# Kernel optimization log

Hardware: AMD Instinct MI355X
Metric: run time of the kernel (lower is better)

The kernel has to match this reference:

```python
import jax, jax.numpy as jnp
import numpy as np
from jax import lax

DN = ('NCHW', 'OIHW', 'NCHW')


def _conv(x, w, pad):
    return lax.conv_general_dilated(x, w, (1, 1), [(pad, pad), (pad, pad)], dimension_numbers=DN)


def _bn(x, gamma, beta, mean, var, eps=1e-5):
    inv = gamma * lax.rsqrt(var + eps)
    return x * inv[None, :, None, None] + (beta - mean * inv)[None, :, None, None]


def _unfold(x, K, pad):
    # torch.nn.Unfold layout: channel-major, kernel positions fastest -> (B, C, K*K, H, W)
    B, C, H, W = x.shape
    p = lax.conv_general_dilated_patches(x, (K, K), (1, 1), [(pad, pad), (pad, pad)], dimension_numbers=DN)
    return p.reshape(B, C, K * K, H, W)


def setup_inputs() -> dict:
    key = jax.random.key(0)
    ks = jax.random.split(key, 16)
    B, C, H, W, K = 16, 64, 64, 64, 3
    d = {
        'x': jax.random.normal(ks[0], (B, C, H, W), jnp.float32),
        'wq': jax.random.normal(ks[1], (C, C, 1, 1), jnp.float32) * 0.1,
        'wk': jax.random.normal(ks[2], (C, C, K, K), jnp.float32) * 0.05,
        'wv': jax.random.normal(ks[3], (C, C, 1, 1), jnp.float32) * 0.1,
        'pos_h': jax.random.normal(ks[4], (C, K, 1), jnp.float32),
        'pos_w': jax.random.normal(ks[5], (C, 1, K), jnp.float32),
    }
    for i, nm in enumerate(['q', 'k', 'v', 'o']):
        d[nm + '_gamma'] = jnp.ones((C,), jnp.float32)
        d[nm + '_beta'] = jnp.zeros((C,), jnp.float32)
        d[nm + '_mean'] = jax.random.normal(ks[6 + i], (C,), jnp.float32) * 0.1
        d[nm + '_var'] = jax.random.uniform(ks[10 + i], (C,), jnp.float32, 0.5, 1.5)
    return d


def reference(x, wq, q_gamma, q_beta, q_mean, q_var,
              wk, k_gamma, k_beta, k_mean, k_var,
              wv, v_gamma, v_beta, v_mean, v_var,
              pos_h, pos_w, o_gamma, o_beta, o_mean, o_var):
    B, C, H, W = x.shape
    K = pos_h.shape[1]
    heads = C // 8
    cph = C // heads  # channels per head

    q = jax.nn.relu(_bn(_conv(x, wq, 0), q_gamma, q_beta, q_mean, q_var))
    k = jax.nn.relu(_bn(_conv(x, wk, K // 2), k_gamma, k_beta, k_mean, k_var))
    v = _bn(_conv(x, wv, 0), v_gamma, v_beta, v_mean, v_var)

    # local keys + positional bias: (B, C, K*K, H, W)
    unfold_k = _unfold(k, K, K // 2)
    pos = (pos_h + pos_w).reshape(1, C, K * K, 1, 1)
    kp = (unfold_k + pos).reshape(B, heads, cph, K * K, H, W)
    qh = q.reshape(B, heads, cph, 1, H, W)

    attn = (qh * kp).sum(axis=2)            # (B, heads, K*K, H, W)
    attn = jax.nn.softmax(attn, axis=2)

    # local aggregation (LocalConvolution): weights shared across cph channels per head
    uv = _unfold(v, K, (K - 1) // 2).reshape(B, heads, cph, K * K, H, W)
    out = (attn[:, :, None] * uv).sum(axis=3).reshape(B, C, H, W)

    out = jax.nn.relu(_bn(out, o_gamma, o_beta, o_mean, o_var))
    return out
```

## Files before the change

### kernel.cpp

```cpp
#include <hip/hip_runtime.h>
#include <hip/hip_bf16.h>
#include <math.h>

#define B_ 16
#define C_ 64
#define H_ 64
#define W_ 64
#define KSTEPS 18

typedef __attribute__((ext_vector_type(8))) short bf16x8;
typedef __attribute__((ext_vector_type(4))) short bf16x4;
typedef __attribute__((ext_vector_type(4))) float f32x4;

static __device__ __forceinline__ unsigned short f2b(float f) {
    __hip_bfloat16 h = __float2bfloat16(f);
    return *reinterpret_cast<unsigned short*>(&h);
}
static __device__ __forceinline__ float b2f(unsigned short u) {
    __hip_bfloat16 h;
    *reinterpret_cast<unsigned short*>(&h) = u;
    return __bfloat162float(h);
}

__global__ __launch_bounds__(64) void prep_kernel(
    const float* __restrict__ wq, const float* __restrict__ wk, const float* __restrict__ wv,
    const float* __restrict__ qg, const float* __restrict__ qb, const float* __restrict__ qm, const float* __restrict__ qv,
    const float* __restrict__ kg, const float* __restrict__ kb, const float* __restrict__ km, const float* __restrict__ kv,
    const float* __restrict__ vg, const float* __restrict__ vb, const float* __restrict__ vm, const float* __restrict__ vv,
    const float* __restrict__ og, const float* __restrict__ ob, const float* __restrict__ om, const float* __restrict__ ov,
    unsigned short* __restrict__ Wp, float* __restrict__ bnp)
{
    const int bid = blockIdx.x;
    const int lane = threadIdx.x;
    if (bid < 12 * KSTEPS) {
        const int mf = bid / KSTEPS;
        const int ks = bid % KSTEPS;
        const int r = lane & 15;
        bf16x8 u;
#pragma unroll
        for (int j = 0; j < 8; j++) {
            int k = ks * 32 + ((lane >> 4) << 3) + j;
            int tap = k >> 6;
            int c = k & 63;
            float w;
            if (mf < 4)      { int co = mf * 16 + r;        w = (tap == 4) ? wq[co * 64 + c] : 0.f; }
            else if (mf < 8) { int co = (mf - 4) * 16 + r;  w = wk[(co * 64 + c) * 9 + tap]; }
            else             { int co = (mf - 8) * 16 + r;  w = (tap == 4) ? wv[co * 64 + c] : 0.f; }
            u[j] = (short)f2b(w);
        }
        *reinterpret_cast<bf16x8*>(Wp + ((size_t)(mf * KSTEPS + ks) * 64 + lane) * 8) = u;
    } else {
        const int c = lane;
        const float* G[4] = {qg, kg, vg, og};
        const float* Bt[4] = {qb, kb, vb, ob};
        const float* M[4] = {qm, km, vm, om};
        const float* V[4] = {qv, kv, vv, ov};
#pragma unroll
        for (int p = 0; p < 4; p++) {
            float inv = G[p][c] * rsqrtf(V[p][c] + 1e-5f);
            bnp[p * 128 + c] = inv;
            bnp[p * 128 + 64 + c] = Bt[p][c] - M[p][c] * inv;
        }
    }
}

__global__ __launch_bounds__(256) void xt_kernel(
    const float* __restrict__ x, unsigned short* __restrict__ xt)
{
    __shared__ float ls[64][65];
    const int b = blockIdx.x >> 6;
    const int h = blockIdx.x & 63;
    const int tid = threadIdx.x;
    const int w = tid & 63;
    const int cg = tid >> 6;
#pragma unroll
    for (int cc = 0; cc < 16; cc++) {
        int c = cg * 16 + cc;
        ls[c][w] = x[((b * 64 + c) * 64 + h) * 64 + w];
    }
    __syncthreads();
    const int px = tid & 63;
    bf16x8 u0, u1;
#pragma unroll
    for (int j = 0; j < 8; j++) {
        u0[j] = (short)f2b(ls[cg * 16 + j][px]);
        u1[j] = (short)f2b(ls[cg * 16 + 8 + j][px]);
    }
    size_t base = ((size_t)((b * 64 + h) * 64 + px)) * 64 + cg * 16;
    *reinterpret_cast<bf16x8*>(xt + base) = u0;
    *reinterpret_cast<bf16x8*>(xt + base + 8) = u1;
}

#define KSM_OFF 0
#define VSM_OFF 25344
#define QSM_OFF 50688
__global__ __launch_bounds__(512, 2) void fused_kernel(
    const unsigned short* __restrict__ xt, const unsigned short* __restrict__ Wp,
    const float* __restrict__ bnp,
    const float* __restrict__ ph, const float* __restrict__ pw,
    float* __restrict__ out)
{
    __shared__ __align__(16) char smem[58880];
    __shared__ float bns[512];
    __shared__ float phs[192], pws[192];
    const int bid = blockIdx.x;
    const int b = bid >> 6;
    const int h = bid & 63;
    const int tid = threadIdx.x;

    for (int i = tid; i < 5 * 66 * 8; i += 512) {
        int ch  = i & 7;
        int col = (i >> 3) % 66;
        int dy  = (i >> 3) / 66;
        int gh = h - 2 + dy, gw = col - 1;
        bf16x8 u = (bf16x8){0,0,0,0,0,0,0,0};
        if ((unsigned)gh < 64u && (unsigned)gw < 64u)
            u = *reinterpret_cast<const bf16x8*>(xt + ((size_t)((b * 64 + gh) * 64 + gw)) * 64 + ch * 8);
        int La = ((dy * 66 + col) * 64 + ch * 8) * 2;
        La ^= (col & 7) << 4;
        *reinterpret_cast<bf16x8*>(smem + La) = u;
    }
    bns[tid & 511] = bnp[tid & 511];
    if (tid < 192) { phs[tid] = ph[tid]; pws[tid] = pw[tid]; }
    __syncthreads();

    const int wid = tid >> 6, lane = tid & 63;
    const int mf = wid & 3, half = wid >> 2;
    const int t = lane & 15, q4 = lane >> 4;
    const int qbase = half ? 0 : 4;

    f32x4 acck[6], accv[6], accq[2];
#pragma unroll
    for (int n = 0; n < 6; n++) { acck[n] = (f32x4){0.f,0.f,0.f,0.f}; accv[n] = (f32x4){0.f,0.f,0.f,0.f}; }
    accq[0] = (f32x4){0.f,0.f,0.f,0.f}; accq[1] = (f32x4){0.f,0.f,0.f,0.f};

#pragma unroll
    for (int ks = 0; ks < KSTEPS; ks++) {
        const int tap = ks >> 1;
        const int dy = tap / 3, dx = tap - dy * 3;
        const int kb = (ks & 1) * 32 + q4 * 8;
        bf16x8 bf[6];
#pragma unroll
        for (int n = 0; n < 6; n++) {
            int p = (half * 6 + n) * 16 + t;
            int r = p >> 6, colw = p & 63;
            int col = colw + dx;
            int La = (((r + dy) * 66 + col) * 64 + kb) * 2;
            La ^= (col & 7) << 4;
            bf[n] = *reinterpret_cast<const bf16x8*>(smem + La);
        }
        bf16x8 afk = *reinterpret_cast<const bf16x8*>(Wp + ((size_t)((4 + mf) * KSTEPS + ks) * 64 + lane) * 8);
#pragma unroll
        for (int n = 0; n < 6; n++)
            acck[n] = __builtin_amdgcn_mfma_f32_16x16x32_bf16(afk, bf[n], acck[n], 0, 0, 0);
        if (ks == 8 || ks == 9) {
            bf16x8 afq = *reinterpret_cast<const bf16x8*>(Wp + ((size_t)(mf * KSTEPS + ks) * 64 + lane) * 8);
            bf16x8 afv = *reinterpret_cast<const bf16x8*>(Wp + ((size_t)((8 + mf) * KSTEPS + ks) * 64 + lane) * 8);
#pragma unroll
            for (int n = 0; n < 6; n++)
                accv[n] = __builtin_amdgcn_mfma_f32_16x16x32_bf16(afv, bf[n], accv[n], 0, 0, 0);
            accq[0] = __builtin_amdgcn_mfma_f32_16x16x32_bf16(afq, bf[qbase], accq[0], 0, 0, 0);
            accq[1] = __builtin_amdgcn_mfma_f32_16x16x32_bf16(afq, bf[qbase + 1], accq[1], 0, 0, 0);
        }
    }
    __syncthreads();

    const int c0 = mf * 16 + q4 * 4;
    {
        f32x4 invk  = *reinterpret_cast<const f32x4*>(&bns[128 + c0]);
        f32x4 biask = *reinterpret_cast<const f32x4*>(&bns[128 + 64 + c0]);
        f32x4 invv  = *reinterpret_cast<const f32x4*>(&bns[256 + c0]);
        f32x4 biasv = *reinterpret_cast<const f32x4*>(&bns[256 + 64 + c0]);
#pragma unroll
        for (int n = 0; n < 6; n++) {
            int p = (half * 6 + n) * 16 + t;
            int r = p >> 6, colw = p & 63;
            int pxp = colw + 1;
            int La = ((r * 66 + pxp) * 64 + c0) * 2;
            La ^= (pxp & 7) << 4;
            bf16x4 pk, pv;
#pragma unroll
            for (int j = 0; j < 4; j++) {
                pk[j] = (short)f2b(fmaxf(acck[n][j] * invk[j] + biask[j], 0.f));
                pv[j] = (short)f2b(accv[n][j] * invv[j] + biasv[j]);
            }
            *reinterpret_cast<bf16x4*>(smem + KSM_OFF + La) = pk;
            *reinterpret_cast<bf16x4*>(smem + VSM_OFF + La) = pv;
        }
        f32x4 invq  = *reinterpret_cast<const f32x4*>(&bns[c0]);
        f32x4 biasq = *reinterpret_cast<const f32x4*>(&bns[64 + c0]);
#pragma unroll
        for (int i = 0; i < 2; i++) {
            int nq = 4 + half * 2 + i;
            int colw = (nq & 3) * 16 + t;
            int La = (colw * 64 + c0) * 2;
            La ^= (colw & 7) << 4;
            bf16x4 pq;
#pragma unroll
            for (int j = 0; j < 4; j++)
                pq[j] = (short)f2b(fmaxf(accq[i][j] * invq[j] + biasq[j], 0.f));
            *reinterpret_cast<bf16x4*>(smem + QSM_OFF + La) = pq;
        }
    }
    __syncthreads();

    const bf16x8 z8 = (bf16x8){0,0,0,0,0,0,0,0};
    for (int i = tid; i < 96; i += 512) {
        int buf = i & 1;
        int j = i >> 1;
        int ch = j & 7;
        int jj = j >> 3;
        int col = (jj & 1) ? 65 : 0;
        int rr = jj >> 1;
        int La = ((rr * 66 + col) * 64 + ch * 8) * 2;
        La ^= (col & 7) << 4;
        *reinterpret_cast<bf16x8*>(smem + (buf ? VSM_OFF : KSM_OFF) + La) = z8;
    }
    int rbad = (h == 0) ? 0 : ((h == 63) ? 2 : -1);
    if (rbad >= 0) {
        for (int i = tid; i < 66 * 8 * 2; i += 512) {
            int buf = i & 1;
            int j = i >> 1;
            int ch = j & 7;
            int col = j >> 3;
            int La = ((rbad * 66 + col) * 64 + ch * 8) * 2;
            La ^= (col & 7) << 4;
            *reinterpret_cast<bf16x8*>(smem + (buf ? VSM_OFF : KSM_OFF) + La) = z8;
        }
    }
    __syncthreads();

    const int px = tid & 63;
    const int head = tid >> 6;
    const int cb = head * 8;

    float qf[8];
    {
        int Lq = (px * 64 + cb) * 2;
        Lq ^= (px & 7) << 4;
        bf16x8 q8 = *reinterpret_cast<const bf16x8*>(smem + QSM_OFF + Lq);
#pragma unroll
        for (int j = 0; j < 8; j++) qf[j] = b2f((unsigned short)q8[j]);
    }

    float A[3], Bx[3];
#pragma unroll
    for (int tt = 0; tt < 3; tt++) {
        float a = 0.f, bb = 0.f;
#pragma unroll
        for (int j = 0; j < 8; j++) {
            a  = fmaf(qf[j], phs[(cb + j) * 3 + tt], a);
            bb = fmaf(qf[j], pws[(cb + j) * 3 + tt], bb);
        }
        A[tt] = a; Bx[tt] = bb;
    }

    float logit[9];
#pragma unroll
    for (int dy = 0; dy < 3; dy++) {
#pragma unroll
        for (int dx = 0; dx < 3; dx++) {
            int pxp = px + dx;
            int La = ((dy * 66 + pxp) * 64 + cb) * 2;
            La ^= (pxp & 7) << 4;
            bf16x8 k8 = *reinterpret_cast<const bf16x8*>(smem + KSM_OFF + La);
            float qk = 0.f;
#pragma unroll
            for (int j = 0; j < 8; j++) qk = fmaf(qf[j], b2f((unsigned short)k8[j]), qk);
            logit[dy * 3 + dx] = qk + A[dy] + Bx[dx];
        }
    }

    float mx = logit[0];
#pragma unroll
    for (int tt = 1; tt < 9; tt++) mx = fmaxf(mx, logit[tt]);
    float e[9], sum = 0.f;
#pragma unroll
    for (int tt = 0; tt < 9; tt++) { e[tt] = __expf(logit[tt] - mx); sum += e[tt]; }
    float inv = 1.f / sum;

    float o[8];
#pragma unroll
    for (int j = 0; j < 8; j++) o[j] = 0.f;
#pragma unroll
    for (int dy = 0; dy < 3; dy++) {
#pragma unroll
        for (int dx = 0; dx < 3; dx++) {
            int pxp = px + dx;
            int La = ((dy * 66 + pxp) * 64 + cb) * 2;
            La ^= (pxp & 7) << 4;
            bf16x8 v8 = *reinterpret_cast<const bf16x8*>(smem + VSM_OFF + La);
            float w = e[dy * 3 + dx];
#pragma unroll
            for (int j = 0; j < 8; j++) o[j] = fmaf(w, b2f((unsigned short)v8[j]), o[j]);
        }
    }

#pragma unroll
    for (int j = 0; j < 8; j++) {
        int c = cb + j;
        float val = fmaxf(fmaf(o[j] * inv, bns[384 + c], bns[384 + 64 + c]), 0.f);
        out[((size_t)(b * C_ + c) * H_ + h) * W_ + px] = val;
    }
}

extern "C" void kernel_launch(void* const* d_in, const int* in_sizes, int n_in,
                              void* d_out, int out_size, void* d_ws, size_t ws_size,
                              hipStream_t stream)
{
    const float* x   = (const float*)d_in[0];
    const float* wq  = (const float*)d_in[1];
    const float* wk  = (const float*)d_in[2];
    const float* wv  = (const float*)d_in[3];
    const float* ph  = (const float*)d_in[4];
    const float* pw  = (const float*)d_in[5];
    const float* qg  = (const float*)d_in[6];
    const float* qb  = (const float*)d_in[7];
    const float* qm  = (const float*)d_in[8];
    const float* qv  = (const float*)d_in[9];
    const float* kg  = (const float*)d_in[10];
    const float* kb  = (const float*)d_in[11];
    const float* km  = (const float*)d_in[12];
    const float* kv  = (const float*)d_in[13];
    const float* vg  = (const float*)d_in[14];
    const float* vb  = (const float*)d_in[15];
    const float* vm  = (const float*)d_in[16];
    const float* vv  = (const float*)d_in[17];
    const float* og  = (const float*)d_in[18];
    const float* ob  = (const float*)d_in[19];
    const float* om  = (const float*)d_in[20];
    const float* ov  = (const float*)d_in[21];

    char* ws = (char*)d_ws;
    unsigned short* Wp = (unsigned short*)ws;
    float* bnp = (float*)(ws + 221184);
    unsigned short* xt = (unsigned short*)(ws + 223232);

    prep_kernel<<<12 * KSTEPS + 1, 64, 0, stream>>>(
        wq, wk, wv, qg, qb, qm, qv, kg, kb, km, kv, vg, vb, vm, vv,
        og, ob, om, ov, Wp, bnp);

    xt_kernel<<<B_ * H_, 256, 0, stream>>>(x, xt);

    fused_kernel<<<B_ * H_, 512, 0, stream>>>(xt, Wp, bnp, ph, pw, (float*)d_out);
}
```

Baseline: 180.3 us.

## Switch shared-memory tiles to channel-chunk-major layout and raise occupancy hint

```diff
diff --git a/kernel.cpp b/kernel.cpp
--- a/kernel.cpp
+++ b/kernel.cpp
@@ -94,7 +94,7 @@
 #define KSM_OFF 0
 #define VSM_OFF 25344
 #define QSM_OFF 50688
-__global__ __launch_bounds__(512, 2) void fused_kernel(
+__global__ __launch_bounds__(512, 4) void fused_kernel(
     const unsigned short* __restrict__ xt, const unsigned short* __restrict__ Wp,
     const float* __restrict__ bnp,
     const float* __restrict__ ph, const float* __restrict__ pw,
@@ -108,17 +108,16 @@
     const int h = bid & 63;
     const int tid = threadIdx.x;
 
-    for (int i = tid; i < 5 * 66 * 8; i += 512) {
-        int ch  = i & 7;
-        int col = (i >> 3) % 66;
-        int dy  = (i >> 3) / 66;
+    for (int i = tid; i < 8 * 5 * 66; i += 512) {
+        int ch   = i & 7;
+        int rest = i >> 3;
+        int col  = rest % 66;
+        int dy   = rest / 66;
         int gh = h - 2 + dy, gw = col - 1;
         bf16x8 u = (bf16x8){0,0,0,0,0,0,0,0};
         if ((unsigned)gh < 64u && (unsigned)gw < 64u)
             u = *reinterpret_cast<const bf16x8*>(xt + ((size_t)((b * 64 + gh) * 64 + gw)) * 64 + ch * 8);
-        int La = ((dy * 66 + col) * 64 + ch * 8) * 2;
-        La ^= (col & 7) << 4;
-        *reinterpret_cast<bf16x8*>(smem + La) = u;
+        *reinterpret_cast<bf16x8*>(smem + ch * 5280 + dy * 1056 + col * 16) = u;
     }
     bns[tid & 511] = bnp[tid & 511];
     if (tid < 192) { phs[tid] = ph[tid]; pws[tid] = pw[tid]; }
@@ -128,6 +127,11 @@
     const int mf = wid & 3, half = wid >> 2;
     const int t = lane & 15, q4 = lane >> 4;
     const int qbase = half ? 0 : 4;
+    const int vb16 = q4 * 5280 + t * 16;
+
+    const unsigned short* WpQ = Wp + (size_t)(mf * KSTEPS) * 512 + lane * 8;
+    const unsigned short* WpK = Wp + (size_t)((4 + mf) * KSTEPS) * 512 + lane * 8;
+    const unsigned short* WpV = Wp + (size_t)((8 + mf) * KSTEPS) * 512 + lane * 8;
 
     f32x4 acck[6], accv[6], accq[2];
 #pragma unroll
@@ -138,24 +142,23 @@
     for (int ks = 0; ks < KSTEPS; ks++) {
         const int tap = ks >> 1;
         const int dy = tap / 3, dx = tap - dy * 3;
-        const int kb = (ks & 1) * 32 + q4 * 8;
+        const int koff = (ks & 1) * 21120;
         bf16x8 bf[6];
 #pragma unroll
         for (int n = 0; n < 6; n++) {
-            int p = (half * 6 + n) * 16 + t;
-            int r = p >> 6, colw = p & 63;
-            int col = colw + dx;
-            int La = (((r + dy) * 66 + col) * 64 + kb) * 2;
-            La ^= (col & 7) << 4;
-            bf[n] = *reinterpret_cast<const bf16x8*>(smem + La);
-        }
-        bf16x8 afk = *reinterpret_cast<const bf16x8*>(Wp + ((size_t)((4 + mf) * KSTEPS + ks) * 64 + lane) * 8);
+            const int n16 = (half * 6 + n) * 16;
+            const int r = n16 >> 6;
+            const int colw0 = n16 & 63;
+            bf[n] = *reinterpret_cast<const bf16x8*>(
+                smem + vb16 + koff + (r + dy) * 1056 + (colw0 + dx) * 16);
+        }
+        bf16x8 afk = *reinterpret_cast<const bf16x8*>(WpK + (size_t)ks * 512);
 #pragma unroll
         for (int n = 0; n < 6; n++)
             acck[n] = __builtin_amdgcn_mfma_f32_16x16x32_bf16(afk, bf[n], acck[n], 0, 0, 0);
         if (ks == 8 || ks == 9) {
-            bf16x8 afq = *reinterpret_cast<const bf16x8*>(Wp + ((size_t)(mf * KSTEPS + ks) * 64 + lane) * 8);
-            bf16x8 afv = *reinterpret_cast<const bf16x8*>(Wp + ((size_t)((8 + mf) * KSTEPS + ks) * 64 + lane) * 8);
+            bf16x8 afq = *reinterpret_cast<const bf16x8*>(WpQ + (size_t)ks * 512);
+            bf16x8 afv = *reinterpret_cast<const bf16x8*>(WpV + (size_t)ks * 512);
 #pragma unroll
             for (int n = 0; n < 6; n++)
                 accv[n] = __builtin_amdgcn_mfma_f32_16x16x32_bf16(afv, bf[n], accv[n], 0, 0, 0);
@@ -166,40 +169,40 @@
     __syncthreads();
 
     const int c0 = mf * 16 + q4 * 4;
+    const int ech = c0 >> 3;
+    const int esub = (q4 & 1) * 8;
     {
         f32x4 invk  = *reinterpret_cast<const f32x4*>(&bns[128 + c0]);
         f32x4 biask = *reinterpret_cast<const f32x4*>(&bns[128 + 64 + c0]);
         f32x4 invv  = *reinterpret_cast<const f32x4*>(&bns[256 + c0]);
         f32x4 biasv = *reinterpret_cast<const f32x4*>(&bns[256 + 64 + c0]);
+        const int ebase = ech * 3168 + esub + t * 16;
 #pragma unroll
         for (int n = 0; n < 6; n++) {
-            int p = (half * 6 + n) * 16 + t;
-            int r = p >> 6, colw = p & 63;
-            int pxp = colw + 1;
-            int La = ((r * 66 + pxp) * 64 + c0) * 2;
-            La ^= (pxp & 7) << 4;
+            const int n16 = (half * 6 + n) * 16;
+            const int r = n16 >> 6;
+            const int colw0 = n16 & 63;
             bf16x4 pk, pv;
 #pragma unroll
             for (int j = 0; j < 4; j++) {
                 pk[j] = (short)f2b(fmaxf(acck[n][j] * invk[j] + biask[j], 0.f));
                 pv[j] = (short)f2b(accv[n][j] * invv[j] + biasv[j]);
             }
-            *reinterpret_cast<bf16x4*>(smem + KSM_OFF + La) = pk;
-            *reinterpret_cast<bf16x4*>(smem + VSM_OFF + La) = pv;
+            const int off = r * 1056 + (colw0 + 1) * 16;
+            *reinterpret_cast<bf16x4*>(smem + KSM_OFF + ebase + off) = pk;
+            *reinterpret_cast<bf16x4*>(smem + VSM_OFF + ebase + off) = pv;
         }
         f32x4 invq  = *reinterpret_cast<const f32x4*>(&bns[c0]);
         f32x4 biasq = *reinterpret_cast<const f32x4*>(&bns[64 + c0]);
+        const int qb16 = QSM_OFF + ech * 1024 + esub + t * 16;
 #pragma unroll
         for (int i = 0; i < 2; i++) {
-            int nq = 4 + half * 2 + i;
-            int colw = (nq & 3) * 16 + t;
-            int La = (colw * 64 + c0) * 2;
-            La ^= (colw & 7) << 4;
+            const int nq = 4 + half * 2 + i;
             bf16x4 pq;
 #pragma unroll
             for (int j = 0; j < 4; j++)
                 pq[j] = (short)f2b(fmaxf(accq[i][j] * invq[j] + biasq[j], 0.f));
-            *reinterpret_cast<bf16x4*>(smem + QSM_OFF + La) = pq;
+            *reinterpret_cast<bf16x4*>(smem + qb16 + (nq & 3) * 256) = pq;
         }
     }
     __syncthreads();
@@ -212,9 +215,8 @@
         int jj = j >> 3;
         int col = (jj & 1) ? 65 : 0;
         int rr = jj >> 1;
-        int La = ((rr * 66 + col) * 64 + ch * 8) * 2;
-        La ^= (col & 7) << 4;
-        *reinterpret_cast<bf16x8*>(smem + (buf ? VSM_OFF : KSM_OFF) + La) = z8;
+        *reinterpret_cast<bf16x8*>(smem + (buf ? VSM_OFF : KSM_OFF)
+                                   + ch * 3168 + rr * 1056 + col * 16) = z8;
     }
     int rbad = (h == 0) ? 0 : ((h == 63) ? 2 : -1);
     if (rbad >= 0) {
@@ -223,9 +225,8 @@
             int j = i >> 1;
             int ch = j & 7;
             int col = j >> 3;
-            int La = ((rbad * 66 + col) * 64 + ch * 8) * 2;
-            La ^= (col & 7) << 4;
-            *reinterpret_cast<bf16x8*>(smem + (buf ? VSM_OFF : KSM_OFF) + La) = z8;
+            *reinterpret_cast<bf16x8*>(smem + (buf ? VSM_OFF : KSM_OFF)
+                                       + ch * 3168 + rbad * 1056 + col * 16) = z8;
         }
     }
     __syncthreads();
@@ -233,12 +234,11 @@
     const int px = tid & 63;
     const int head = tid >> 6;
     const int cb = head * 8;
+    const int abase = head * 3168 + px * 16;
 
     float qf[8];
     {
-        int Lq = (px * 64 + cb) * 2;
-        Lq ^= (px & 7) << 4;
-        bf16x8 q8 = *reinterpret_cast<const bf16x8*>(smem + QSM_OFF + Lq);
+        bf16x8 q8 = *reinterpret_cast<const bf16x8*>(smem + QSM_OFF + head * 1024 + px * 16);
 #pragma unroll
         for (int j = 0; j < 8; j++) qf[j] = b2f((unsigned short)q8[j]);
     }
@@ -260,10 +260,8 @@
     for (int dy = 0; dy < 3; dy++) {
 #pragma unroll
         for (int dx = 0; dx < 3; dx++) {
-            int pxp = px + dx;
-            int La = ((dy * 66 + pxp) * 64 + cb) * 2;
-            La ^= (pxp & 7) << 4;
-            bf16x8 k8 = *reinterpret_cast<const bf16x8*>(smem + KSM_OFF + La);
+            bf16x8 k8 = *reinterpret_cast<const bf16x8*>(
+                smem + KSM_OFF + abase + dy * 1056 + dx * 16);
             float qk = 0.f;
 #pragma unroll
             for (int j = 0; j < 8; j++) qk = fmaf(qf[j], b2f((unsigned short)k8[j]), qk);
@@ -286,10 +284,8 @@
     for (int dy = 0; dy < 3; dy++) {
 #pragma unroll
         for (int dx = 0; dx < 3; dx++) {
-            int pxp = px + dx;
-            int La = ((dy * 66 + pxp) * 64 + cb) * 2;
-            La ^= (pxp & 7) << 4;
-            bf16x8 v8 = *reinterpret_cast<const bf16x8*>(smem + VSM_OFF + La);
+            bf16x8 v8 = *reinterpret_cast<const bf16x8*>(
+                smem + VSM_OFF + abase + dy * 1056 + dx * 16);
             float w = e[dy * 3 + dx];
 #pragma unroll
             for (int j = 0; j < 8; j++) o[j] = fmaf(w, b2f((unsigned short)v8[j]), o[j]);
```

Result: slower. 234.6 us (+30.1%).
